# Kernel optimization log

Measured on AMD Instinct MI355X. Metric: run time of the kernel, lower is better.

## Reference

```python
import jax, jax.numpy as jnp
import numpy as np

N_LAYER = 4
N_HEAD = 8
D_HEAD = 64
D_MODEL = 512
D_INNER = 2048
NMT = 16  # num_mem_tokens
BSZ = 1
QLEN = 2048


def _rel_shift(x):
    # x: [i, j, b, n] -> Transformer-XL relative shift
    i, j, b, n = x.shape
    zero_pad = jnp.zeros((i, 1, b, n), dtype=x.dtype)
    x_padded = jnp.concatenate([zero_pad, x], axis=1)  # [i, j+1, b, n]
    x_padded = x_padded.reshape(j + 1, i, b, n)
    return x_padded[1:].reshape(i, j, b, n)


def _layer_norm(x, g, b):
    mu = jnp.mean(x, axis=-1, keepdims=True)
    var = jnp.mean(jnp.square(x - mu), axis=-1, keepdims=True)
    return (x - mu) / jnp.sqrt(var + 1e-5) * g + b


def setup_inputs() -> dict:
    key = jax.random.key(0)
    ks = jax.random.split(key, 12)
    s = 0.02
    return {
        "word_emb": jax.random.normal(ks[0], (BSZ, QLEN, D_MODEL), jnp.float32),
        "mem_tokens": jax.random.normal(ks[1], (NMT, BSZ, D_MODEL), jnp.float32),
        "Wqkv": jax.random.normal(ks[2], (N_LAYER, D_MODEL, 3 * N_HEAD * D_HEAD), jnp.float32) * s,
        "Wr": jax.random.normal(ks[3], (N_LAYER, D_MODEL, N_HEAD * D_HEAD), jnp.float32) * s,
        "Wo": jax.random.normal(ks[4], (N_LAYER, N_HEAD * D_HEAD, D_MODEL), jnp.float32) * s,
        "ln1_scale": jnp.ones((N_LAYER, D_MODEL), jnp.float32),
        "ln1_bias": jnp.zeros((N_LAYER, D_MODEL), jnp.float32),
        "ffn_W1": jax.random.normal(ks[5], (N_LAYER, D_MODEL, D_INNER), jnp.float32) * s,
        "ffn_b1": jnp.zeros((N_LAYER, D_INNER), jnp.float32),
        "ffn_W2": jax.random.normal(ks[6], (N_LAYER, D_INNER, D_MODEL), jnp.float32) * s,
        "ffn_b2": jnp.zeros((N_LAYER, D_MODEL), jnp.float32),
        "ln2_scale": jnp.ones((N_LAYER, D_MODEL), jnp.float32),
        "ln2_bias": jnp.zeros((N_LAYER, D_MODEL), jnp.float32),
        "r_w_bias": jax.random.normal(ks[7], (N_HEAD, D_HEAD), jnp.float32) * s,
        "r_r_bias": jax.random.normal(ks[8], (N_HEAD, D_HEAD), jnp.float32) * s,
    }


def reference(word_emb, mem_tokens, Wqkv, Wr, Wo, ln1_scale, ln1_bias,
              ffn_W1, ffn_b1, ffn_W2, ffn_b2, ln2_scale, ln2_bias,
              r_w_bias, r_r_bias):
    # word_emb: [B, Q, D] -> [Q, B, D]; prepend + append mem tokens (mem_at_end)
    w = jnp.transpose(word_emb, (1, 0, 2))
    w = jnp.concatenate([mem_tokens, w, mem_tokens], axis=0)  # [T, B, D]
    T, B = w.shape[0], w.shape[1]

    # causal mask (mlen=0) with mem-token exceptions, True = masked
    mask = jnp.triu(jnp.ones((T, T), dtype=bool), k=1)
    mask = mask.at[:NMT, :NMT].set(False)          # read-mem block attends to itself
    mask = mask.at[-NMT:, -NMT:].set(False)        # write-mem block attends to itself

    # sinusoidal relative positional embedding, pos_seq = T-1 .. 0
    inv_freq = 1.0 / (10000.0 ** (jnp.arange(0, D_MODEL, 2, dtype=jnp.float32) / D_MODEL))
    pos_seq = jnp.arange(T - 1, -1, -1.0, dtype=jnp.float32)
    sinusoid = pos_seq[:, None] * inv_freq[None, :]
    pos_emb = jnp.concatenate([jnp.sin(sinusoid), jnp.cos(sinusoid)], axis=-1)  # [T, D]

    scale = 1.0 / np.sqrt(D_HEAD)
    for l in range(N_LAYER):
        heads = w @ Wqkv[l]                                        # [T, B, 3*H*Dh]
        q, k, v = jnp.split(heads, 3, axis=-1)
        q = q.reshape(T, B, N_HEAD, D_HEAD)
        k = k.reshape(T, B, N_HEAD, D_HEAD)
        v = v.reshape(T, B, N_HEAD, D_HEAD)
        r = (pos_emb @ Wr[l]).reshape(T, N_HEAD, D_HEAD)           # [T, H, Dh]

        AC = jnp.einsum('ibnd,jbnd->ijbn', q + r_w_bias, k)
        BD = _rel_shift(jnp.einsum('ibnd,jnd->ijbn', q + r_r_bias, r))
        score = (AC + BD) * scale                                  # [T, T, B, H]
        score = jnp.where(mask[:, :, None, None], -1e30, score)
        prob = jax.nn.softmax(score, axis=1)
        attn_vec = jnp.einsum('ijbn,jbnd->ibnd', prob, v).reshape(T, B, N_HEAD * D_HEAD)

        w = _layer_norm(w + attn_vec @ Wo[l], ln1_scale[l], ln1_bias[l])  # post-LN
        ff = jax.nn.relu(w @ ffn_W1[l] + ffn_b1[l]) @ ffn_W2[l] + ffn_b2[l]
        w = _layer_norm(w + ff, ln2_scale[l], ln2_bias[l])
    return w  # [T, B, D]
```

## Files before the change

kernel.cpp:

```cpp
#include <hip/hip_runtime.h>
#include <hip/hip_bf16.h>
#include <math.h>
#include <stdint.h>

#define TT 2080
#define DM 512
#define DI 2048
#define NH 8
#define DH 64
#define NMTOK 16
#define NLAYER 4
#define QKV_N 1536
#define ATT_SCALE 0.125f
#define NCH 4
#define WT_STRIDE 3407872
#define BDF_HEAD 2196480
#define WRAP_HEAD 33280

typedef short bf16x8 __attribute__((ext_vector_type(8)));
typedef float f32x4 __attribute__((ext_vector_type(4)));
typedef unsigned short ushort_t;

__device__ __forceinline__ ushort_t f2bf(float f) {
  __hip_bfloat16 h = __float2bfloat16(f);
  return *reinterpret_cast<ushort_t*>(&h);
}
__device__ __forceinline__ float bfbits2f(unsigned int hi_bits) {
  return __uint_as_float(hi_bits);
}
__device__ __forceinline__ float bf2f(ushort_t u) {
  return bfbits2f(((unsigned int)u) << 16);
}
__device__ __forceinline__ void unpack8(uint4 v, float* f) {
  f[0] = bfbits2f(v.x << 16); f[1] = bfbits2f(v.x & 0xffff0000u);
  f[2] = bfbits2f(v.y << 16); f[3] = bfbits2f(v.y & 0xffff0000u);
  f[4] = bfbits2f(v.z << 16); f[5] = bfbits2f(v.z & 0xffff0000u);
  f[6] = bfbits2f(v.w << 16); f[7] = bfbits2f(v.w & 0xffff0000u);
}
__device__ __forceinline__ unsigned int pack2(ushort_t lo, ushort_t hi) {
  return (unsigned int)lo | ((unsigned int)hi << 16);
}
__device__ __forceinline__ void barrier_lds() {
  asm volatile("s_waitcnt lgkmcnt(0)" ::: "memory");
  __builtin_amdgcn_s_barrier();
}
__device__ __forceinline__ void gload16(const ushort_t* g, ushort_t* l) {
  __builtin_amdgcn_global_load_lds(
      (__attribute__((address_space(1))) void*)(uintptr_t)g,
      (__attribute__((address_space(3))) void*)(uintptr_t)l, 16, 0, 0);
}
__device__ __forceinline__ size_t ft512(int r, int c) {
  return (((size_t)(r >> 4) * 16 + (c >> 5)) << 9) + (((c >> 3) & 3) << 7) +
         ((r & 15) << 3) + (c & 7);
}

__global__ __launch_bounds__(256) void k_prep(
    const float* __restrict__ Wqkv, const float* __restrict__ Wr,
    const float* __restrict__ Wo, const float* __restrict__ W1,
    const float* __restrict__ W2, ushort_t* __restrict__ dstAll,
    const float* __restrict__ we, const float* __restrict__ mem,
    float* __restrict__ w, ushort_t* __restrict__ wbft,
    ushort_t* __restrict__ posft) {
  const int tid = threadIdx.x;
  if (blockIdx.x >= 13312) {
    int idx = (blockIdx.x - 13312) * 256 + tid;
    if (idx >= TT * DM) return;
    int t = idx >> 9, d = idx & 511;
    float v;
    if (t < NMTOK) v = mem[t * DM + d];
    else if (t < NMTOK + 2048) v = we[(t - NMTOK) * DM + d];
    else v = mem[(t - (NMTOK + 2048)) * DM + d];
    w[idx] = v;
    wbft[ft512(t, d)] = f2bf(v);
    float p = (float)(TT - 1 - t);
    int i2 = d & 255;
    float freq = __expf(-0.035977892f * (float)i2);
    float ang = p * freq;
    posft[ft512(t, d)] = f2bf((d < 256) ? __sinf(ang) : __cosf(ang));
    return;
  }
  __shared__ float tl[32][33];
  const int l = blockIdx.x / 3328;
  int idx = blockIdx.x % 3328;
  const float* src;
  ushort_t* dst = dstAll + (size_t)l * WT_STRIDE;
  int K, N, local;
  bool isFT = true;
  if (idx < 768)       { src = Wqkv + (size_t)l * 512 * 1536; K = 512;  N = 1536; local = idx; }
  else if (idx < 1024) { src = Wr   + (size_t)l * 512 * 512;  dst += 786432;  K = 512;  N = 512;  local = idx - 768; }
  else if (idx < 1280) { src = Wo   + (size_t)l * 512 * 512;  dst += 1048576; K = 512;  N = 512;  local = idx - 1024; isFT = false; }
  else if (idx < 2304) { src = W1   + (size_t)l * 512 * 2048; dst += 1310720; K = 512;  N = 2048; local = idx - 1280; }
  else                 { src = W2   + (size_t)l * 2048 * 512; dst += 2359296; K = 2048; N = 512;  local = idx - 2304; }
  const int ntiles = N / 32;
  const int n0 = (local % ntiles) * 32, k0 = (local / ntiles) * 32;
#pragma unroll
  for (int p = 0; p < 4; ++p) {
    int row = (tid >> 5) + 8 * p, col = tid & 31;
    tl[row][col] = src[(size_t)(k0 + row) * N + n0 + col];
  }
  __syncthreads();
  if (isFT) {
    if (tid < 128) {
      int b = tid >> 6, l2 = tid & 63;
      int nn = b * 16 + (l2 & 15);
      int kq = (l2 >> 4) * 8;
      ushort_t t8[8];
#pragma unroll
      for (int e = 0; e < 8; ++e) t8[e] = f2bf(tl[kq + e][nn]);
      size_t ad = (((size_t)((n0 >> 4) + b) * (K >> 5) + (k0 >> 5)) << 9) +
                  ((size_t)l2 << 3);
      *(uint4*)&dst[ad] = *(uint4*)t8;
    }
  } else {
#pragma unroll
    for (int p = 0; p < 4; ++p) {
      int n = (tid >> 5) + 8 * p, k = tid & 31;
      dst[(size_t)(n0 + n) * K + k0 + k] = f2bf(tl[k][n]);
    }
  }
}

__device__ __forceinline__ void gemm32x64_body(const ushort_t* __restrict__ A,
                                               const ushort_t* __restrict__ Bt,
                                               const float* __restrict__ bias,
                                               float* __restrict__ C,
                                               ushort_t* __restrict__ Cb,
                                               int N, int K, int flags,
                                               int m0, int n0) {
  __shared__ short As[32][72];
  __shared__ short Bs[64][72];
  const int tid = threadIdx.x;
  const int lane = tid & 63, wv = tid >> 6;
  const int wm = (wv >> 1) * 16, wn = (wv & 1) * 32;
  const int lm = lane & 15, quad = lane >> 4;
  const int sr = tid >> 3, sc8 = (tid & 7) * 8;

  f32x4 acc[2];
  acc[0] = (f32x4)(0.f); acc[1] = (f32x4)(0.f);

  auto loadA = [&](int k0) -> uint4 {
    return *(const uint4*)&A[(size_t)(m0 + sr) * K + k0 + sc8];
  };
  auto loadB = [&](int row, int k0) -> uint4 {
    return *(const uint4*)&Bt[(size_t)(n0 + row) * K + k0 + sc8];
  };

  uint4 aC = loadA(0), b0C = loadB(sr, 0), b1C = loadB(sr + 32, 0);

  for (int k0 = 0; k0 < K; k0 += 64) {
    const int kn = (k0 + 64 < K) ? k0 + 64 : k0;
    uint4 aN = loadA(kn), b0N = loadB(sr, kn), b1N = loadB(sr + 32, kn);
    barrier_lds();
    *(uint4*)&As[sr][sc8] = aC;
    *(uint4*)&Bs[sr][sc8] = b0C;
    *(uint4*)&Bs[sr + 32][sc8] = b1C;
    barrier_lds();
#pragma unroll
    for (int kk = 0; kk < 64; kk += 32) {
      bf16x8 a = *(const bf16x8*)&As[wm + lm][kk + quad * 8];
      bf16x8 b0 = *(const bf16x8*)&Bs[wn + lm][kk + quad * 8];
      bf16x8 b1 = *(const bf16x8*)&Bs[wn + 16 + lm][kk + quad * 8];
      acc[0] = __builtin_amdgcn_mfma_f32_16x16x32_bf16(a, b0, acc[0], 0, 0, 0);
      acc[1] = __builtin_amdgcn_mfma_f32_16x16x32_bf16(a, b1, acc[1], 0, 0, 0);
    }
    aC = aN; b0C = b0N; b1C = b1N;
  }
#pragma unroll
  for (int nt = 0; nt < 2; ++nt) {
    int col = n0 + wn + nt * 16 + lm;
    float bv = (flags & 1) ? bias[col] : 0.f;
#pragma unroll
    for (int t = 0; t < 4; ++t) {
      int row = m0 + wm + quad * 4 + t;
      float v = acc[nt][t] + bv;
      if (flags & 2) v = fmaxf(v, 0.f);
      if (flags & 4) Cb[(size_t)row * N + col] = f2bf(v);
      else C[(size_t)row * N + col] = v;
    }
  }
}

__global__ __launch_bounds__(256) void k_gemm_mfma(const ushort_t* __restrict__ A,
                                                   const ushort_t* __restrict__ Bt,
                                                   const float* __restrict__ bias,
                                                   float* __restrict__ C,
                                                   ushort_t* __restrict__ Cb,
                                                   int N, int K, int flags) {
  gemm32x64_body(A, Bt, bias, C, Cb, N, K, flags, blockIdx.y * 32, blockIdx.x * 64);
}

__device__ __forceinline__ void gemm_ft_body(
    ushort_t* smem, const ushort_t* __restrict__ A, const ushort_t* __restrict__ Bt,
    const float* __restrict__ bias, int N, int K, int kBeg, int kEnd,
    int m0, int n0, int flags, int omode,
    float* __restrict__ Cf, ushort_t* __restrict__ Cb, int cftKT,
    ushort_t* __restrict__ aux, const float* __restrict__ rwb,
    const float* __restrict__ rrb) {
  const int tid = threadIdx.x;
  const int lane = tid & 63, wv = tid >> 6;
  const int wm = (wv >> 1) * 32, wn = (wv & 1) * 64;
  const int lm = lane & 15, quad = lane >> 4;
  const int AKT = K >> 5;
  const int mt0 = m0 >> 4, nt0 = n0 >> 4;
  const int kt0 = kBeg >> 5;

  f32x4 acc[2][4];
#pragma unroll
  for (int i = 0; i < 2; ++i)
#pragma unroll
    for (int j = 0; j < 4; ++j) acc[i][j] = (f32x4)(0.f);

  auto stage = [&](ushort_t* dA, int ktg) {
    ushort_t* dB = dA + 4096;
#pragma unroll
    for (int it = 0; it < 6; ++it) {
      const int c = (it << 8) + tid;
      if (it < 2) {
        const int blk = c >> 6, ln = c & 63;
        gload16(A + (((size_t)(mt0 + (blk >> 1)) * AKT + ktg + (blk & 1)) << 9) + (ln << 3),
                dA + (c << 3));
      } else {
        const int cB = c - 512;
        const int blk = cB >> 6, ln = cB & 63;
        gload16(Bt + (((size_t)(nt0 + (blk >> 1)) * AKT + ktg + (blk & 1)) << 9) + (ln << 3),
                dB + (cB << 3));
      }
    }
  };
  auto compute = [&](const ushort_t* dA) {
    const ushort_t* dB = dA + 4096;
#pragma unroll
    for (int kk = 0; kk < 2; ++kk) {
      bf16x8 a[2], b[4];
#pragma unroll
      for (int i = 0; i < 2; ++i)
        a[i] = *(const bf16x8*)&dA[((((wm >> 4) + i) << 1) + kk) * 512 + (lane << 3)];
#pragma unroll
      for (int j = 0; j < 4; ++j)
        b[j] = *(const bf16x8*)&dB[((((wn >> 4) + j) << 1) + kk) * 512 + (lane << 3)];
#pragma unroll
      for (int i = 0; i < 2; ++i)
#pragma unroll
        for (int j = 0; j < 4; ++j)
          acc[i][j] = __builtin_amdgcn_mfma_f32_16x16x32_bf16(a[i], b[j], acc[i][j], 0, 0, 0);
    }
  };

  const int nIter = (kEnd - kBeg) >> 6;
  stage(smem, kt0);
  __syncthreads();
  for (int t = 0; t < nIter; t += 2) {
    if (t + 1 < nIter) stage(smem + 12288, kt0 + (t + 1) * 2);
    compute(smem);
    __syncthreads();
    if (t + 2 < nIter) stage(smem, kt0 + (t + 2) * 2);
    compute(smem + 12288);
    __syncthreads();
  }

#pragma unroll
  for (int i = 0; i < 2; ++i) {
    const int rowb = m0 + wm + i * 16 + quad * 4;
#pragma unroll
    for (int j = 0; j < 4; ++j) {
      const int col = n0 + wn + j * 16 + lm;
      const float bv = (flags & 1) ? bias[col] : 0.f;
#pragma unroll
      for (int t2 = 0; t2 < 4; ++t2) {
        const int row = rowb + t2;
        float v = acc[i][j][t2] + bv;
        if (flags & 2) v = fmaxf(v, 0.f);
        if (omode == 0) {
          Cf[(size_t)row * N + col] = v;
        } else if (omode == 1) {
          Cb[(size_t)row * N + col] = f2bf(v);
        } else if (omode == 2) {
          Cb[(((size_t)(row >> 4) * cftKT + (col >> 5)) << 9) +
             (((col >> 3) & 3) << 7) + ((row & 15) << 3) + (col & 7)] = f2bf(v);
        } else if (omode == 3) {
          Cb[ft512(row, col)] = f2bf(v + rwb[col]);
          aux[(size_t)row * DM + col] = f2bf(v + rrb[col]);
        } else if (omode == 4) {
          Cb[ft512(row, col - 512)] = f2bf(v);
        } else {
          const int dv = col - 1024;
          Cb[((size_t)(dv >> 4) * 65 + (row >> 5)) * 512 +
             (((row >> 3) & 3) << 7) + ((dv & 15) << 3) + (row & 7)] = f2bf(v);
        }
      }
    }
  }
}

__global__ __launch_bounds__(256) void k_gemm_qkvwr_ft(
    const ushort_t* __restrict__ wbft, const ushort_t* __restrict__ posft,
    const ushort_t* __restrict__ qkvT, const ushort_t* __restrict__ wrT,
    ushort_t* __restrict__ qwft, ushort_t* __restrict__ kft,
    ushort_t* __restrict__ vtft, ushort_t* __restrict__ rbg,
    ushort_t* __restrict__ qrb, const float* __restrict__ rwb,
    const float* __restrict__ rrb) {
  __shared__ ushort_t smem[24576];
  int m0 = blockIdx.y * 64;
  if (m0 + 64 > TT) m0 = TT - 64;
  const int bx = blockIdx.x;
  if (bx < 12) {
    const int om = (bx < 4) ? 3 : (bx < 8 ? 4 : 5);
    ushort_t* dst = (om == 3) ? qwft : (om == 4) ? kft : vtft;
    gemm_ft_body(smem, wbft, qkvT, nullptr, QKV_N, DM, 0, DM, m0, bx * 128,
                 0, om, nullptr, dst, 0, qrb, rwb, rrb);
  } else {
    gemm_ft_body(smem, posft, wrT, nullptr, DM, DM, 0, DM, m0, (bx - 12) * 128,
                 0, 1, nullptr, rbg, 0, nullptr, nullptr, nullptr);
  }
}

__global__ __launch_bounds__(256) void k_ffn1_ft(const ushort_t* __restrict__ wbft,
                                                 const ushort_t* __restrict__ w1T,
                                                 const float* __restrict__ b1l,
                                                 ushort_t* __restrict__ ff1ft) {
  __shared__ ushort_t smem[24576];
  int m0 = blockIdx.y * 64;
  if (m0 + 64 > TT) m0 = TT - 64;
  gemm_ft_body(smem, wbft, w1T, b1l, DI, DM, 0, DM, m0, blockIdx.x * 128,
               1 | 2, 2, nullptr, ff1ft, DI >> 5, nullptr, nullptr, nullptr);
}

__global__ __launch_bounds__(256) void k_ffn2_ft(const ushort_t* __restrict__ ff1ft,
                                                 const ushort_t* __restrict__ w2T,
                                                 const float* __restrict__ b2l,
                                                 float* __restrict__ ff2p) {
  __shared__ ushort_t smem[24576];
  int m0 = blockIdx.y * 64;
  if (m0 + 64 > TT) m0 = TT - 64;
  const int s = blockIdx.z;
  gemm_ft_body(smem, ff1ft, w2T, b2l, DM, DI, s * 512, s * 512 + 512, m0,
               blockIdx.x * 128, (s == 0) ? 1 : 0, 0,
               ff2p + (size_t)s * TT * DM, nullptr, 0, nullptr, nullptr, nullptr);
}

__global__ __launch_bounds__(256) void k_qr(const ushort_t* __restrict__ qrb,
                                            const ushort_t* __restrict__ rbg,
                                            ushort_t* __restrict__ bdf,
                                            ushort_t* __restrict__ wrapv) {
  const int h = blockIdx.z;
  const int m0 = blockIdx.y * 32, n0 = blockIdx.x * 64;
  if (!(n0 == 0 || n0 + 63 >= TT - 32 - m0)) return;
  __shared__ short As[32][72];
  __shared__ short Bs[64][72];
  const int tid = threadIdx.x;
  const int lane = tid & 63, wv = tid >> 6;
  const int wm = (wv >> 1) * 16, wn = (wv & 1) * 32;
  const int lm = lane & 15, quad = lane >> 4;
  const int sr = tid >> 3, sc8 = (tid & 7) * 8;
  const uint4 zero4 = make_uint4(0, 0, 0, 0);

  *(uint4*)&As[sr][sc8] = *(const uint4*)&qrb[(size_t)(m0 + sr) * DM + h * DH + sc8];
  int br0 = n0 + sr, br1 = n0 + sr + 32;
  *(uint4*)&Bs[sr][sc8] =
      (br0 < TT) ? *(const uint4*)&rbg[(size_t)br0 * DM + h * DH + sc8] : zero4;
  *(uint4*)&Bs[sr + 32][sc8] =
      (br1 < TT) ? *(const uint4*)&rbg[(size_t)br1 * DM + h * DH + sc8] : zero4;
  __syncthreads();

  f32x4 acc[2];
  acc[0] = (f32x4)(0.f); acc[1] = (f32x4)(0.f);
#pragma unroll
  for (int kk = 0; kk < 64; kk += 32) {
    bf16x8 a = *(const bf16x8*)&As[wm + lm][kk + quad * 8];
    bf16x8 b0 = *(const bf16x8*)&Bs[wn + lm][kk + quad * 8];
    bf16x8 b1 = *(const bf16x8*)&Bs[wn + 16 + lm][kk + quad * 8];
    acc[0] = __builtin_amdgcn_mfma_f32_16x16x32_bf16(a, b0, acc[0], 0, 0, 0);
    acc[1] = __builtin_amdgcn_mfma_f32_16x16x32_bf16(a, b1, acc[1], 0, 0, 0);
  }
  const size_t hb = (size_t)h * BDF_HEAD;
  const size_t hw = (size_t)h * WRAP_HEAD;
#pragma unroll
  for (int nt = 0; nt < 2; ++nt) {
    int col = n0 + wn + nt * 16 + lm;
    if (col >= TT) continue;
#pragma unroll
    for (int t = 0; t < 4; ++t) {
      int row = m0 + wm + quad * 4 + t;
      float v = acc[nt][t];
      ushort_t vb = f2bf(v);
      int p = row + col - (TT - 1);
      if (p >= 0) {
        int qti = row >> 5, jti = p >> 5;
        int ri = row & 31, cj = p & 31;
        size_t tb = hb + (((size_t)(qti * (qti + 1) / 2 + jti)) << 10);
        size_t off = (size_t)((((ri >> 4) * 2 + (cj >> 4)) << 8) +
                              ((((ri & 15) >> 2) * 16 + (cj & 15)) << 2) + (ri & 3));
        bdf[tb + off] = vb;
      }
      if (col < 16) wrapv[hw + row * 16 + col] = vb;
    }
  }
}

__global__ __launch_bounds__(256) void k_attn(const ushort_t* __restrict__ qwft,
                                              const ushort_t* __restrict__ kft,
                                              const ushort_t* __restrict__ vtft,
                                              const ushort_t* __restrict__ bdf,
                                              const ushort_t* __restrict__ wrapv,
                                              float* __restrict__ mlP,
                                              ushort_t* __restrict__ opP) {
  const int h = blockIdx.y;
  const int qt = 64 - blockIdx.x;
  const int tid = threadIdx.x;
  const int wv = tid >> 6;
  if (wv > qt) return;
  const int lane = tid & 63;
  const int lm = lane & 15, quad = lane >> 4;
  const int i0 = qt * 32;

  __shared__ ushort_t pbl[4][1024];

  bf16x8 qf[2][2];
#pragma unroll
  for (int qi = 0; qi < 2; ++qi)
#pragma unroll
    for (int kt = 0; kt < 2; ++kt)
      qf[qi][kt] = *(const bf16x8*)&qwft[(((size_t)((i0 >> 4) + qi) * 16) +
                                         h * 2 + kt) * 512 + (lane << 3)];

  const size_t hbd = (size_t)h * BDF_HEAD + (((size_t)(qt * (qt + 1) / 2)) << 10);
  const size_t hwr = (size_t)h * WRAP_HEAD;

  float mreg[2][4], lreg[2][4];
#pragma unroll
  for (int qi = 0; qi < 2; ++qi)
#pragma unroll
    for (int t = 0; t < 4; ++t) { mreg[qi][t] = -INFINITY; lreg[qi][t] = 0.f; }
  f32x4 o[4][2];
#pragma unroll
  for (int dt = 0; dt < 4; ++dt)
#pragma unroll
    for (int iq = 0; iq < 2; ++iq) o[dt][iq] = (f32x4)(0.f);

  for (int jt = wv; jt <= qt; jt += NCH) {
    const int j0 = jt * 32;
    bf16x8 kf[2][2];
#pragma unroll
    for (int jq = 0; jq < 2; ++jq)
#pragma unroll
      for (int kt = 0; kt < 2; ++kt)
        kf[jq][kt] = *(const bf16x8*)&kft[(((size_t)((j0 >> 4) + jq) * 16) +
                                          h * 2 + kt) * 512 + (lane << 3)];
    bf16x8 vf[4];
#pragma unroll
    for (int dt = 0; dt < 4; ++dt)
      vf[dt] = *(const bf16x8*)&vtft[(((size_t)(h * 4 + dt)) * 65 + jt) * 512 +
                                     (lane << 3)];
    uint2 bd[2][2];
#pragma unroll
    for (int qi = 0; qi < 2; ++qi)
#pragma unroll
      for (int jq = 0; jq < 2; ++jq)
        bd[qi][jq] = *(const uint2*)&bdf[hbd + ((size_t)jt << 10) +
                                         ((qi * 2 + jq) << 8) + (lane << 2)];

    f32x4 sA[2][2];
#pragma unroll
    for (int qi = 0; qi < 2; ++qi)
#pragma unroll
      for (int jq = 0; jq < 2; ++jq) {
        f32x4 ac = (f32x4)(0.f);
#pragma unroll
        for (int kt = 0; kt < 2; ++kt)
          ac = __builtin_amdgcn_mfma_f32_16x16x32_bf16(qf[qi][kt], kf[jq][kt], ac, 0, 0, 0);
        sA[qi][jq] = ac;
      }

    if (jt < qt) {
#pragma unroll
      for (int qi = 0; qi < 2; ++qi)
#pragma unroll
        for (int jq = 0; jq < 2; ++jq) {
          float b0 = bf2f((ushort_t)(bd[qi][jq].x & 0xffffu));
          float b1 = bf2f((ushort_t)(bd[qi][jq].x >> 16));
          float b2 = bf2f((ushort_t)(bd[qi][jq].y & 0xffffu));
          float b3 = bf2f((ushort_t)(bd[qi][jq].y >> 16));
          sA[qi][jq][0] = (sA[qi][jq][0] + b0) * ATT_SCALE;
          sA[qi][jq][1] = (sA[qi][jq][1] + b1) * ATT_SCALE;
          sA[qi][jq][2] = (sA[qi][jq][2] + b2) * ATT_SCALE;
          sA[qi][jq][3] = (sA[qi][jq][3] + b3) * ATT_SCALE;
        }
    } else {
#pragma unroll
      for (int qi = 0; qi < 2; ++qi)
#pragma unroll
        for (int jq = 0; jq < 2; ++jq) {
          float bdv[4];
          bdv[0] = bf2f((ushort_t)(bd[qi][jq].x & 0xffffu));
          bdv[1] = bf2f((ushort_t)(bd[qi][jq].x >> 16));
          bdv[2] = bf2f((ushort_t)(bd[qi][jq].y & 0xffffu));
          bdv[3] = bf2f((ushort_t)(bd[qi][jq].y >> 16));
          const int j = j0 + jq * 16 + lm;
#pragma unroll
          for (int t = 0; t < 4; ++t) {
            const int i = i0 + qi * 16 + quad * 4 + t;
            const float acv = sA[qi][jq][t];
            float s;
            if (j <= i) {
              s = (acv + bdv[t]) * ATT_SCALE;
            } else {
              bool inmem = (i < NMTOK && j < NMTOK) ||
                           (i >= TT - NMTOK && j >= TT - NMTOK);
              if (!inmem) s = -1e30f;
              else if (j == i + 1) s = acv * ATT_SCALE;
              else s = (acv + bf2f(wrapv[hwr + (i + 1) * 16 + (j - i - 2)])) * ATT_SCALE;
            }
            sA[qi][jq][t] = s;
          }
        }
    }

    float mx[2][4];
#pragma unroll
    for (int qi = 0; qi < 2; ++qi)
#pragma unroll
      for (int t = 0; t < 4; ++t)
        mx[qi][t] = fmaxf(sA[qi][0][t], sA[qi][1][t]);
#pragma unroll
    for (int off = 1; off < 16; off <<= 1)
#pragma unroll
      for (int qi = 0; qi < 2; ++qi)
#pragma unroll
        for (int t = 0; t < 4; ++t)
          mx[qi][t] = fmaxf(mx[qi][t], __shfl_xor(mx[qi][t], off));
    float al[2][4];
#pragma unroll
    for (int qi = 0; qi < 2; ++qi)
#pragma unroll
      for (int t = 0; t < 4; ++t) {
        float mnew = fmaxf(mreg[qi][t], mx[qi][t]);
        al[qi][t] = __expf(mreg[qi][t] - mnew);
        mreg[qi][t] = mnew;
      }
    float ps[2][4];
#pragma unroll
    for (int qi = 0; qi < 2; ++qi)
#pragma unroll
      for (int t = 0; t < 4; ++t) {
        sA[qi][0][t] = __expf(sA[qi][0][t] - mreg[qi][t]);
        sA[qi][1][t] = __expf(sA[qi][1][t] - mreg[qi][t]);
        ps[qi][t] = sA[qi][0][t] + sA[qi][1][t];
      }
#pragma unroll
    for (int off = 1; off < 16; off <<= 1)
#pragma unroll
      for (int qi = 0; qi < 2; ++qi)
#pragma unroll
        for (int t = 0; t < 4; ++t)
          ps[qi][t] += __shfl_xor(ps[qi][t], off);
#pragma unroll
    for (int qi = 0; qi < 2; ++qi)
#pragma unroll
      for (int t = 0; t < 4; ++t)
        lreg[qi][t] = lreg[qi][t] * al[qi][t] + ps[qi][t];

    float aw[2];
    {
      const int src = (lm >> 2) << 4;
      const int t3 = lm & 3;
#pragma unroll
      for (int iq = 0; iq < 2; ++iq) {
        float g0 = __shfl(al[iq][0], src);
        float g1 = __shfl(al[iq][1], src);
        float g2 = __shfl(al[iq][2], src);
        float g3 = __shfl(al[iq][3], src);
        aw[iq] = (t3 == 0) ? g0 : (t3 == 1) ? g1 : (t3 == 2) ? g2 : g3;
      }
    }
#pragma unroll
    for (int dt = 0; dt < 4; ++dt)
#pragma unroll
      for (int iq = 0; iq < 2; ++iq)
#pragma unroll
        for (int tt = 0; tt < 4; ++tt) o[dt][iq][tt] *= aw[iq];

#pragma unroll
    for (int qi = 0; qi < 2; ++qi)
#pragma unroll
      for (int jq = 0; jq < 2; ++jq)
#pragma unroll
        for (int t = 0; t < 4; ++t)
          pbl[wv][(qi << 9) +
                  (((jq * 2 + (lm >> 3)) * 16 + (quad * 4 + t)) << 3) +
                  (lm & 7)] = f2bf(sA[qi][jq][t]);
    asm volatile("s_waitcnt lgkmcnt(0)" ::: "memory");
    __builtin_amdgcn_sched_barrier(0);
    bf16x8 pf[2];
#pragma unroll
    for (int iq = 0; iq < 2; ++iq)
      pf[iq] = *(const bf16x8*)&pbl[wv][(iq << 9) + (lane << 3)];

#pragma unroll
    for (int dt = 0; dt < 4; ++dt)
#pragma unroll
      for (int iq = 0; iq < 2; ++iq)
        o[dt][iq] = __builtin_amdgcn_mfma_f32_16x16x32_bf16(vf[dt], pf[iq], o[dt][iq], 0, 0, 0);
  }

  const int pidx = (qt * NH + h) * NCH + wv;
  if (lm == 0) {
#pragma unroll
    for (int qi = 0; qi < 2; ++qi)
#pragma unroll
      for (int t = 0; t < 4; ++t) {
        mlP[(size_t)pidx * 64 + qi * 16 + quad * 4 + t] = mreg[qi][t];
        mlP[(size_t)pidx * 64 + 32 + qi * 16 + quad * 4 + t] = lreg[qi][t];
      }
  }
  const size_t ob = (size_t)pidx * 2048;
#pragma unroll
  for (int iq = 0; iq < 2; ++iq)
#pragma unroll
    for (int dt = 0; dt < 4; ++dt) {
      ushort_t o4[4];
#pragma unroll
      for (int tt = 0; tt < 4; ++tt) o4[tt] = f2bf(o[dt][iq][tt]);
      *(uint2*)&opP[ob + (size_t)(iq * 16 + lm) * 64 + dt * 16 + quad * 4] =
          *(uint2*)o4;
    }
}

__global__ __launch_bounds__(256) void k_attn_combine(const float* __restrict__ mlP,
                                                      const ushort_t* __restrict__ opP,
                                                      ushort_t* __restrict__ attnb) {
  const int qt = blockIdx.x, h = blockIdx.y;
  const int nc = (qt + 1 < NCH) ? qt + 1 : NCH;
  const int tid = threadIdx.x;
  const int i = tid >> 3, d8 = (tid & 7) * 8;
  const size_t base = (size_t)(qt * NH + h) * NCH;
  float m[NCH], l[NCH], wgt[NCH];
  float M = -INFINITY;
  for (int cc = 0; cc < nc; ++cc) {
    m[cc] = mlP[(base + cc) * 64 + i];
    l[cc] = mlP[(base + cc) * 64 + 32 + i];
    M = fmaxf(M, m[cc]);
  }
  float L = 0.f;
  for (int cc = 0; cc < nc; ++cc) { wgt[cc] = __expf(m[cc] - M); L += l[cc] * wgt[cc]; }
  float acc[8] = {0, 0, 0, 0, 0, 0, 0, 0};
  for (int cc = 0; cc < nc; ++cc) {
    uint4 v = *(const uint4*)&opP[(base + cc) * 2048 + (size_t)i * 64 + d8];
    float f[8]; unpack8(v, f);
#pragma unroll
    for (int k = 0; k < 8; ++k) acc[k] += wgt[cc] * f[k];
  }
  const float inv = 1.f / L;
  ushort_t o8[8];
#pragma unroll
  for (int k = 0; k < 8; ++k) o8[k] = f2bf(acc[k] * inv);
  *(uint4*)&attnb[(size_t)(qt * 32 + i) * DM + h * DH + d8] = *(uint4*)o8;
}

__global__ __launch_bounds__(256) void k_addln(const float* __restrict__ w,
                                               float* __restrict__ wout,
                                               ushort_t* __restrict__ wbft,
                                               const float* __restrict__ delta,
                                               int nparts,
                                               const float* __restrict__ gamma,
                                               const float* __restrict__ beta) {
  const int row = blockIdx.x;
  const int tid = threadIdx.x;
  __shared__ float red[4], red2[4];
  __shared__ float sm[512];
  size_t base = (size_t)row * DM;
  float x0 = w[base + tid];
  float x1 = w[base + tid + 256];
  for (int p = 0; p < nparts; ++p) {
    x0 += delta[(size_t)p * TT * DM + base + tid];
    x1 += delta[(size_t)p * TT * DM + base + tid + 256];
  }
  float s = x0 + x1;
#pragma unroll
  for (int off = 1; off < 64; off <<= 1) s += __shfl_xor(s, off);
  if ((tid & 63) == 0) red[tid >> 6] = s;
  __syncthreads();
  float mu = (red[0] + red[1] + red[2] + red[3]) * (1.f / 512.f);
  float d0 = x0 - mu, d1 = x1 - mu;
  float v = d0 * d0 + d1 * d1;
#pragma unroll
  for (int off = 1; off < 64; off <<= 1) v += __shfl_xor(v, off);
  if ((tid & 63) == 0) red2[tid >> 6] = v;
  __syncthreads();
  float var = (red2[0] + red2[1] + red2[2] + red2[3]) * (1.f / 512.f);
  float rstd = rsqrtf(var + 1e-5f);
  float o0 = d0 * rstd * gamma[tid] + beta[tid];
  float o1 = d1 * rstd * gamma[tid + 256] + beta[tid + 256];
  wout[base + tid] = o0;
  wout[base + tid + 256] = o1;
  sm[tid] = o0; sm[tid + 256] = o1;
  __syncthreads();
  if (tid < 64) {
    const int d8 = tid << 3;
    ushort_t t8[8];
#pragma unroll
    for (int e = 0; e < 8; ++e) t8[e] = f2bf(sm[d8 + e]);
    *(uint4*)&wbft[ft512(row, d8)] = *(uint4*)t8;
  }
}

extern "C" void kernel_launch(void* const* d_in, const int* in_sizes, int n_in,
                              void* d_out, int out_size, void* d_ws, size_t ws_size,
                              hipStream_t stream) {
  const float* we   = (const float*)d_in[0];
  const float* mem  = (const float*)d_in[1];
  const float* Wqkv = (const float*)d_in[2];
  const float* Wr   = (const float*)d_in[3];
  const float* Wo   = (const float*)d_in[4];
  const float* ln1s = (const float*)d_in[5];
  const float* ln1b = (const float*)d_in[6];
  const float* W1   = (const float*)d_in[7];
  const float* b1   = (const float*)d_in[8];
  const float* W2   = (const float*)d_in[9];
  const float* b2   = (const float*)d_in[10];
  const float* ln2s = (const float*)d_in[11];
  const float* ln2b = (const float*)d_in[12];
  const float* rwb  = (const float*)d_in[13];
  const float* rrb  = (const float*)d_in[14];

  float* w     = (float*)d_ws;
  float* proj  = w + (size_t)TT * DM;
  ushort_t* wbft  = (ushort_t*)(proj + (size_t)TT * DM);
  ushort_t* posft = wbft + (size_t)TT * DM;
  ushort_t* attnb = posft + (size_t)TT * DM;
  ushort_t* qkvB  = attnb + (size_t)TT * DM;
  ushort_t* qwft  = qkvB;
  ushort_t* kft   = qkvB + (size_t)TT * DM;
  ushort_t* vtft  = qkvB + (size_t)2 * TT * DM;
  ushort_t* rbg   = qkvB + (size_t)TT * QKV_N;
  ushort_t* WtAll = rbg + (size_t)TT * DM;
  ushort_t* opP   = WtAll + (size_t)NLAYER * WT_STRIDE;
  float* mlP   = (float*)(opP + (size_t)65 * 8 * 8 * 2048);
  ushort_t* qrb  = (ushort_t*)(mlP + (size_t)65 * 8 * 8 * 64);
  ushort_t* bdf  = qrb + (size_t)TT * DM;
  ushort_t* wrapv = attnb;
  ushort_t* ff1ft = qkvB;
  float* ff2p  = (float*)opP;
  const size_t OFF_QKVT = 0, OFF_WRT = 786432, OFF_WOT = 1048576,
               OFF_W1T = 1310720, OFF_W2T = 2359296;

  k_prep<<<13312 + 4160, 256, 0, stream>>>(Wqkv, Wr, Wo, W1, W2, WtAll,
                                           we, mem, w, wbft, posft);

  dim3 gQW(16, 33);
  dim3 gW1(16, 33);
  dim3 gW2(4, 33, 4);
  dim3 gDM32(DM / 64, 65);
  dim3 gQR(33, 65, NH);
  dim3 gA(65, NH);
  dim3 gC(65, NH);

  for (int l = 0; l < NLAYER; ++l) {
    const ushort_t* Wt = WtAll + (size_t)l * WT_STRIDE;
    k_gemm_qkvwr_ft<<<gQW, 256, 0, stream>>>(wbft, posft, Wt + OFF_QKVT,
                                             Wt + OFF_WRT, qwft, kft, vtft,
                                             rbg, qrb, rwb, rrb);
    k_qr<<<gQR, 256, 0, stream>>>(qrb, rbg, bdf, wrapv);
    k_attn<<<gA, 256, 0, stream>>>(qwft, kft, vtft, bdf, wrapv, mlP, opP);
    k_attn_combine<<<gC, 256, 0, stream>>>(mlP, opP, attnb);
    k_gemm_mfma<<<gDM32, 256, 0, stream>>>(attnb, Wt + OFF_WOT, nullptr, proj, nullptr,
                                           DM, DM, 0);
    k_addln<<<TT, 256, 0, stream>>>(w, w, wbft, proj, 1,
                                    ln1s + (size_t)l * DM, ln1b + (size_t)l * DM);
    k_ffn1_ft<<<gW1, 256, 0, stream>>>(wbft, Wt + OFF_W1T, b1 + (size_t)l * DI, ff1ft);
    k_ffn2_ft<<<gW2, 256, 0, stream>>>(ff1ft, Wt + OFF_W2T, b2 + (size_t)l * DM, ff2p);
    float* wout = (l == NLAYER - 1) ? (float*)d_out : w;
    k_addln<<<TT, 256, 0, stream>>>(w, wout, wbft, ff2p, 4,
                                    ln2s + (size_t)l * DM, ln2b + (size_t)l * DM);
  }
}
```

Baseline: 676.2 us.

## Split attention KV loop over eight chunks and prefetch next K/BD tiles

The attention kernel's key-tile loop is now split across two blocks per (query tile, head) along a new grid z dimension, giving eight partial chunks instead of four. The combine kernel is updated to merge up to eight partial softmax results. Inside the loop, the K fragments and relative-position bias for the next iteration are loaded before the current tile's softmax and PV work, to hide global load latency. This adds more partial outputs for the combine step to merge and raises register pressure from the double-buffered fragments.

```diff
diff --git a/kernel.cpp b/kernel.cpp
--- a/kernel.cpp
+++ b/kernel.cpp
@@ -12,7 +12,7 @@
 #define NLAYER 4
 #define QKV_N 1536
 #define ATT_SCALE 0.125f
-#define NCH 4
+#define NCHT 8
 #define WT_STRIDE 3407872
 #define BDF_HEAD 2196480
 #define WRAP_HEAD 33280
@@ -408,7 +408,8 @@
   const int qt = 64 - blockIdx.x;
   const int tid = threadIdx.x;
   const int wv = tid >> 6;
-  if (wv > qt) return;
+  const int cid = blockIdx.z * 4 + wv;
+  if (cid > qt) return;
   const int lane = tid & 63;
   const int lm = lane & 15, quad = lane >> 4;
   const int i0 = qt * 32;
@@ -426,38 +427,44 @@
   const size_t hbd = (size_t)h * BDF_HEAD + (((size_t)(qt * (qt + 1) / 2)) << 10);
   const size_t hwr = (size_t)h * WRAP_HEAD;
 
-  float mreg[2][4], lreg[2][4];
-#pragma unroll
-  for (int qi = 0; qi < 2; ++qi)
-#pragma unroll
-    for (int t = 0; t < 4; ++t) { mreg[qi][t] = -INFINITY; lreg[qi][t] = 0.f; }
-  f32x4 o[4][2];
-#pragma unroll
-  for (int dt = 0; dt < 4; ++dt)
-#pragma unroll
-    for (int iq = 0; iq < 2; ++iq) o[dt][iq] = (f32x4)(0.f);
-
-  for (int jt = wv; jt <= qt; jt += NCH) {
+  auto loadKB = [&](int jt, bf16x8 (&kf)[2][2], uint2 (&bd)[2][2]) {
     const int j0 = jt * 32;
-    bf16x8 kf[2][2];
 #pragma unroll
     for (int jq = 0; jq < 2; ++jq)
 #pragma unroll
       for (int kt = 0; kt < 2; ++kt)
         kf[jq][kt] = *(const bf16x8*)&kft[(((size_t)((j0 >> 4) + jq) * 16) +
                                           h * 2 + kt) * 512 + (lane << 3)];
+#pragma unroll
+    for (int qi = 0; qi < 2; ++qi)
+#pragma unroll
+      for (int jq = 0; jq < 2; ++jq)
+        bd[qi][jq] = *(const uint2*)&bdf[hbd + ((size_t)jt << 10) +
+                                         ((qi * 2 + jq) << 8) + (lane << 2)];
+  };
+
+  float mreg[2][4], lreg[2][4];
+#pragma unroll
+  for (int qi = 0; qi < 2; ++qi)
+#pragma unroll
+    for (int t = 0; t < 4; ++t) { mreg[qi][t] = -INFINITY; lreg[qi][t] = 0.f; }
+  f32x4 o[4][2];
+#pragma unroll
+  for (int dt = 0; dt < 4; ++dt)
+#pragma unroll
+    for (int iq = 0; iq < 2; ++iq) o[dt][iq] = (f32x4)(0.f);
+
+  bf16x8 kf[2][2];
+  uint2 bd[2][2];
+  loadKB(cid, kf, bd);
+
+  for (int jt = cid; jt <= qt; jt += NCHT) {
+    const int j0 = jt * 32;
     bf16x8 vf[4];
 #pragma unroll
     for (int dt = 0; dt < 4; ++dt)
       vf[dt] = *(const bf16x8*)&vtft[(((size_t)(h * 4 + dt)) * 65 + jt) * 512 +
                                      (lane << 3)];
-    uint2 bd[2][2];
-#pragma unroll
-    for (int qi = 0; qi < 2; ++qi)
-#pragma unroll
-      for (int jq = 0; jq < 2; ++jq)
-        bd[qi][jq] = *(const uint2*)&bdf[hbd + ((size_t)jt << 10) +
-                                         ((qi * 2 + jq) << 8) + (lane << 2)];
 
     f32x4 sA[2][2];
 #pragma unroll
@@ -470,6 +477,11 @@
           ac = __builtin_amdgcn_mfma_f32_16x16x32_bf16(qf[qi][kt], kf[jq][kt], ac, 0, 0, 0);
         sA[qi][jq] = ac;
       }
+
+    const int jn = (jt + NCHT <= qt) ? jt + NCHT : jt;
+    bf16x8 kn[2][2];
+    uint2 bdn[2][2];
+    loadKB(jn, kn, bdn);
 
     if (jt < qt) {
 #pragma unroll
@@ -600,9 +612,18 @@
 #pragma unroll
       for (int iq = 0; iq < 2; ++iq)
         o[dt][iq] = __builtin_amdgcn_mfma_f32_16x16x32_bf16(vf[dt], pf[iq], o[dt][iq], 0, 0, 0);
-  }
-
-  const int pidx = (qt * NH + h) * NCH + wv;
+
+#pragma unroll
+    for (int jq = 0; jq < 2; ++jq)
+#pragma unroll
+      for (int kt = 0; kt < 2; ++kt) kf[jq][kt] = kn[jq][kt];
+#pragma unroll
+    for (int qi = 0; qi < 2; ++qi)
+#pragma unroll
+      for (int jq = 0; jq < 2; ++jq) bd[qi][jq] = bdn[qi][jq];
+  }
+
+  const int pidx = (qt * NH + h) * NCHT + cid;
   if (lm == 0) {
 #pragma unroll
     for (int qi = 0; qi < 2; ++qi)
@@ -629,11 +650,11 @@
                                                       const ushort_t* __restrict__ opP,
                                                       ushort_t* __restrict__ attnb) {
   const int qt = blockIdx.x, h = blockIdx.y;
-  const int nc = (qt + 1 < NCH) ? qt + 1 : NCH;
+  const int nc = (qt + 1 < NCHT) ? qt + 1 : NCHT;
   const int tid = threadIdx.x;
   const int i = tid >> 3, d8 = (tid & 7) * 8;
-  const size_t base = (size_t)(qt * NH + h) * NCH;
-  float m[NCH], l[NCH], wgt[NCH];
+  const size_t base = (size_t)(qt * NH + h) * NCHT;
+  float m[NCHT], l[NCHT], wgt[NCHT];
   float M = -INFINITY;
   for (int cc = 0; cc < nc; ++cc) {
     m[cc] = mlP[(base + cc) * 64 + i];
@@ -751,7 +772,7 @@
   dim3 gW2(4, 33, 4);
   dim3 gDM32(DM / 64, 65);
   dim3 gQR(33, 65, NH);
-  dim3 gA(65, NH);
+  dim3 gA(65, NH, 2);
   dim3 gC(65, NH);
 
   for (int l = 0; l < NLAYER; ++l) {
```

Result: no change. 665.4 us (-1.6%).
